# Performance work log

Hardware: AMD Instinct MI355X
Metric: run time of the kernel (lower is better)

Reference implementation:

```python
import jax, jax.numpy as jnp
import numpy as np

GROUP_SIZE = 128
N_BITS = 4
QMAX = 2 ** N_BITS - 1
NUM_EXPERTS = 8
HIDDEN = 2048
INTER = 768
NUM_ROT = 4
T_TOKENS = 4096
TOP_K = 2


def _make_pairs(rng, n_rot, in_feat):
    # intra-group permutation per rotation (valid disjoint Givens pairs)
    n_groups = in_feat // GROUP_SIZE
    return np.stack([
        np.concatenate([rng.permutation(GROUP_SIZE) for _ in range(n_groups)])
        for _ in range(n_rot)
    ]).astype(np.int32)


def _round_ste(x):
    return x + jax.lax.stop_gradient(jnp.round(x) - x)


def _rotate(W, pairs, angles):
    # W: [N, in_feat]; pairs: [R, in_feat] intra-group perm; angles: [R, in_feat//2]
    in_feat = W.shape[1]
    base = (jnp.arange(in_feat) // GROUP_SIZE) * GROUP_SIZE
    for r in range(pairs.shape[0]):
        abs_idx = base + pairs[r]
        i_idx = abs_idx[0::2]
        j_idx = abs_idx[1::2]
        c = jnp.cos(angles[r])
        s = jnp.sin(angles[r])
        wi = W[:, i_idx]
        wj = W[:, j_idx]
        W = W.at[:, i_idx].set(c * wi - s * wj).at[:, j_idx].set(s * wi + c * wj)
    return W


def _fake_quant(W):
    # groupwise asymmetric min-max fake quantization with STE rounding
    shape = W.shape
    wg = W.reshape(-1, GROUP_SIZE)
    wmax = wg.max(axis=-1, keepdims=True)
    wmin = wg.min(axis=-1, keepdims=True)
    scale = jnp.clip(wmax - wmin, 1e-5, None) / QMAX
    zero = jnp.round(-wmin / scale)
    q = jnp.clip(_round_ste(wg / scale) + zero, 0.0, float(QMAX))
    return ((q - zero) * scale).reshape(shape)


def _pseudo_quantize(W3, pairs, angles, ch_scales):
    # scale -> rotate -> fake-quant -> inverse rotate (reversed order, -angles) -> unscale
    E, O, In = W3.shape
    W = W3.reshape(-1, In) * ch_scales
    W = _rotate(W, pairs, angles)
    W = _fake_quant(W)
    W = _rotate(W, pairs[::-1], -angles[::-1])
    return (W / ch_scales).reshape(E, O, In)


def setup_inputs() -> dict:
    key = jax.random.key(0)
    ks = jax.random.split(key, 8)
    rng = np.random.default_rng(0)
    hidden_states = jax.random.normal(ks[0], (T_TOKENS, HIDDEN), jnp.float32)
    top_k_index = jax.random.randint(ks[1], (T_TOKENS, TOP_K), 0, NUM_EXPERTS, jnp.int32)
    logits = jax.random.normal(ks[2], (T_TOKENS, TOP_K), jnp.float32)
    top_k_weights = jax.nn.softmax(logits, axis=-1)
    gate_up_weight = jax.random.normal(ks[3], (NUM_EXPERTS, 2 * INTER, HIDDEN), jnp.float32) * 0.02
    down_weight = jax.random.normal(ks[4], (NUM_EXPERTS, HIDDEN, INTER), jnp.float32) * 0.02
    gate_up_pairs = jnp.asarray(_make_pairs(rng, NUM_ROT, HIDDEN))
    down_pairs = jnp.asarray(_make_pairs(rng, NUM_ROT, INTER))
    gate_up_angles = jax.random.normal(ks[5], (NUM_ROT, HIDDEN // 2), jnp.float32) * 0.1
    down_angles = jax.random.normal(ks[6], (NUM_ROT, INTER // 2), jnp.float32) * 0.1
    k7, k8 = jax.random.split(ks[7])
    gate_up_channel_scales = jax.random.uniform(k7, (1, HIDDEN), jnp.float32, 0.5, 1.5)
    down_channel_scales = jax.random.uniform(k8, (1, INTER), jnp.float32, 0.5, 1.5)
    return {
        "hidden_states": hidden_states,
        "top_k_index": top_k_index,
        "top_k_weights": top_k_weights,
        "gate_up_weight": gate_up_weight,
        "down_weight": down_weight,
        "gate_up_pairs": gate_up_pairs,
        "gate_up_angles": gate_up_angles,
        "down_pairs": down_pairs,
        "down_angles": down_angles,
        "gate_up_channel_scales": gate_up_channel_scales,
        "down_channel_scales": down_channel_scales,
    }


def reference(hidden_states, top_k_index, top_k_weights, gate_up_weight, down_weight,
              gate_up_pairs, gate_up_angles, down_pairs, down_angles,
              gate_up_channel_scales, down_channel_scales):
    # dequantize expert weights
    gup = _pseudo_quantize(gate_up_weight, gate_up_pairs, gate_up_angles, gate_up_channel_scales)  # [E,2I,H]
    dwn = _pseudo_quantize(down_weight, down_pairs, down_angles, down_channel_scales)              # [E,H,I]
    T = hidden_states.shape[0]
    E = gup.shape[0]
    # dense dispatch: all experts for all tokens (E small), combined by routing weights
    h = jnp.einsum('th,eoh->teo', hidden_states, gup)          # [T,E,2I]
    gate, up = jnp.split(h, 2, axis=-1)
    inter = jax.nn.silu(gate) * up                              # [T,E,I]
    y = jnp.einsum('tei,ehi->teh', inter, dwn)                  # [T,E,H]
    combine = jnp.zeros((T, E), hidden_states.dtype)
    combine = combine.at[jnp.arange(T)[:, None], top_k_index].add(top_k_weights)
    return jnp.einsum('teh,te->th', y, combine)
```

## Files before the change

### kernel.cpp

```cpp
#include <hip/hip_runtime.h>

#define T_TOKENS 4096
#define HIDDEN   2048
#define INTERM   768
#define NE       8
#define NPAIR    8192
#define NROT     4
#define MAXT     40

typedef __bf16 bf16x8 __attribute__((ext_vector_type(8)));
typedef float  f32x4  __attribute__((ext_vector_type(4)));

__device__ __forceinline__ unsigned short f2bf(float f) {
  unsigned u = __float_as_uint(f);
  u += 0x7fffu + ((u >> 16) & 1u);
  return (unsigned short)(u >> 16);
}

__device__ __forceinline__ void async16(const void* g, void* l) {
  __builtin_amdgcn_global_load_lds((const __attribute__((address_space(1))) void*)g,
                                   (__attribute__((address_space(3))) void*)l, 16, 0, 0);
}

__global__ void k_hist(const int* __restrict__ idx, int* __restrict__ cnt) {
  const int t = blockIdx.x * 256 + threadIdx.x;
  if (t < NPAIR) atomicAdd(&cnt[idx[t]], 1);
}

__global__ void k_scan(const int* __restrict__ cnt, int* __restrict__ off,
                       int* __restrict__ cur, int* __restrict__ tmap,
                       int* __restrict__ nv) {
  if (threadIdx.x == 0) {
    int a = 0, tt = 0;
    for (int e = 0; e < NE; ++e) {
      off[e] = a; cur[e] = 0;
      const int c = cnt[e];
      for (int m = 0; m < c; m += 256) tmap[tt++] = (e << 16) | (m >> 8);
      a += c;
    }
    nv[0] = tt;
    for (; tt < MAXT; ++tt) tmap[tt] = -1;
  }
}

__global__ void k_scatter(const int* __restrict__ idx, const float* __restrict__ wts,
                          const int* __restrict__ off, int* __restrict__ cur,
                          int* __restrict__ pt, float* __restrict__ pw) {
  const int t = blockIdx.x * 256 + threadIdx.x;
  if (t < NPAIR) {
    const int e = idx[t];
    const int pos = off[e] + atomicAdd(&cur[e], 1);
    pt[pos] = t;
    pw[pos] = wts[t];
  }
}

__global__ void k_tbl(const int* __restrict__ gp, const float* __restrict__ ga,
                      const int* __restrict__ dp, const float* __restrict__ da,
                      const float* __restrict__ gch, const float* __restrict__ dch,
                      float4* __restrict__ tg, float4* __restrict__ td,
                      float* __restrict__ grch, float* __restrict__ drch) {
  const int t = blockIdx.x * 256 + threadIdx.x;
  if (t < NROT * (HIDDEN / 2)) {
    const int r = t >> 10, s = t & 1023;
    const int grp = s >> 6;
    const int i = gp[r * HIDDEN + 2 * s], j = gp[r * HIDDEN + 2 * s + 1];
    const float a = ga[r * (HIDDEN / 2) + s];
    const float c = cosf(a), sn = sinf(a);
    tg[(grp * NROT + r) * 128 + i] = make_float4(c, -sn, __int_as_float(j), 0.f);
    tg[(grp * NROT + r) * 128 + j] = make_float4(c,  sn, __int_as_float(i), 0.f);
  }
  if (t < NROT * (INTERM / 2)) {
    const int r = t / (INTERM / 2), s = t - r * (INTERM / 2);
    const int grp = s >> 6;
    const int i = dp[r * INTERM + 2 * s], j = dp[r * INTERM + 2 * s + 1];
    const float a = da[r * (INTERM / 2) + s];
    const float c = cosf(a), sn = sinf(a);
    td[(grp * NROT + r) * 128 + i] = make_float4(c, -sn, __int_as_float(j), 0.f);
    td[(grp * NROT + r) * 128 + j] = make_float4(c,  sn, __int_as_float(i), 0.f);
  }
  if (t < HIDDEN) grch[t] = 1.0f / gch[t];
  if (t < INTERM) drch[t] = 1.0f / dch[t];
}

#define FWD_ROT(tl, v0, v1)                                                     \
  _Pragma("unroll")                                                             \
  for (int r = 0; r < NROT; ++r) {                                              \
    const float4 e0 = tl[r * 128 + l];                                          \
    const float4 e1 = tl[r * 128 + 64 + l];                                     \
    const int p0 = __float_as_int(e0.z), p1 = __float_as_int(e1.z);             \
    const int a0 = (p0 & 63) << 2, a1 = (p1 & 63) << 2;                         \
    _Pragma("unroll")                                                           \
    for (int q = 0; q < 4; ++q) {                                               \
      const int x0 = __float_as_int(v0[q]), x1 = __float_as_int(v1[q]);         \
      const float lo0 = __int_as_float(__builtin_amdgcn_ds_bpermute(a0, x0));   \
      const float hi0 = __int_as_float(__builtin_amdgcn_ds_bpermute(a0, x1));   \
      const float lo1 = __int_as_float(__builtin_amdgcn_ds_bpermute(a1, x0));   \
      const float hi1 = __int_as_float(__builtin_amdgcn_ds_bpermute(a1, x1));   \
      const float op0 = (p0 & 64) ? hi0 : lo0;                                  \
      const float op1 = (p1 & 64) ? hi1 : lo1;                                  \
      {                                                                         \
        _Pragma("clang fp contract(off)")                                       \
        v0[q] = e0.x * v0[q] + e0.y * op0;                                      \
        v1[q] = e1.x * v1[q] + e1.y * op1;                                      \
      }                                                                         \
    }                                                                           \
  }

__global__ __launch_bounds__(256) void k_quant(
    const float* __restrict__ W, const float4* __restrict__ tbl,
    const float* __restrict__ ch, unsigned short* __restrict__ out, int In, int G) {
  __shared__ float4 tl[NROT * 128];
  const int wv = threadIdx.x >> 6, l = threadIdx.x & 63;
  const int g = blockIdx.x % G;
  const int rowblk = blockIdx.x / G;
  const int row0 = rowblk * 16 + wv * 4;
  const int colbase = g << 7;
  tl[threadIdx.x]       = tbl[(size_t)g * NROT * 128 + threadIdx.x];
  tl[256 + threadIdx.x] = tbl[(size_t)g * NROT * 128 + 256 + threadIdx.x];
  __syncthreads();
  const float c0 = ch[colbase + l], c1 = ch[colbase + 64 + l];
  float v0[4], v1[4];
#pragma unroll
  for (int q = 0; q < 4; ++q) {
#pragma clang fp contract(off)
    const float* Wr = W + (size_t)(row0 + q) * In + colbase;
    v0[q] = Wr[l] * c0;
    v1[q] = Wr[64 + l] * c1;
  }
  FWD_ROT(tl, v0, v1)
#pragma unroll
  for (int q = 0; q < 4; ++q) {
    float mn = fminf(v0[q], v1[q]), mx = fmaxf(v0[q], v1[q]);
#pragma unroll
    for (int o = 32; o > 0; o >>= 1) {
      mn = fminf(mn, __shfl_xor(mn, o));
      mx = fmaxf(mx, __shfl_xor(mx, o));
    }
    {
#pragma clang fp contract(off)
      const float scale = fmaxf(mx - mn, 1e-5f) / 15.0f;
      const float zero = rintf(-mn / scale);
      const float q0 = fminf(fmaxf(rintf(v0[q] / scale) + zero, 0.0f), 15.0f);
      const float q1 = fminf(fmaxf(rintf(v1[q] / scale) + zero, 0.0f), 15.0f);
      v0[q] = (q0 - zero) * scale;
      v1[q] = (q1 - zero) * scale;
    }
  }
#pragma unroll
  for (int q = 0; q < 4; ++q) {
    unsigned short* Or = out + (size_t)(row0 + q) * In + colbase;
    Or[l]      = f2bf(v0[q]);
    Or[64 + l] = f2bf(v1[q]);
  }
}

__global__ __launch_bounds__(256) void k_rotx(
    const float* __restrict__ X, const float* __restrict__ rch,
    const float4* __restrict__ tbl, unsigned short* __restrict__ out) {
  __shared__ float4 tl[NROT * 128];
  const int wv = threadIdx.x >> 6, l = threadIdx.x & 63;
  const int g = blockIdx.x % 16;
  const int rowblk = blockIdx.x / 16;
  const int row0 = rowblk * 16 + wv * 4;
  const int colbase = g << 7;
  tl[threadIdx.x]       = tbl[(size_t)g * NROT * 128 + threadIdx.x];
  tl[256 + threadIdx.x] = tbl[(size_t)g * NROT * 128 + 256 + threadIdx.x];
  __syncthreads();
  const float i0 = rch[colbase + l], i1 = rch[colbase + 64 + l];
  float v0[4], v1[4];
#pragma unroll
  for (int q = 0; q < 4; ++q) {
    const float* Xr = X + (size_t)(row0 + q) * HIDDEN + colbase;
    v0[q] = Xr[l] * i0;
    v1[q] = Xr[64 + l] * i1;
  }
  FWD_ROT(tl, v0, v1)
#pragma unroll
  for (int q = 0; q < 4; ++q) {
    unsigned short* Or = out + (size_t)(row0 + q) * HIDDEN + colbase;
    Or[l]      = f2bf(v0[q]);
    Or[64 + l] = f2bf(v1[q]);
  }
}

__global__ __launch_bounds__(256) void k_silu2(
    const float* __restrict__ h, const float* __restrict__ pw,
    const float* __restrict__ rch, const float4* __restrict__ tbl,
    unsigned short* __restrict__ out) {
  __shared__ float4 tl[NROT * 128];
  const int wv = threadIdx.x >> 6, l = threadIdx.x & 63;
  const int g = blockIdx.x % 6;
  const int rowblk = blockIdx.x / 6;
  const int row0 = rowblk * 16 + wv * 4;
  const int colbase = g << 7;
  tl[threadIdx.x]       = tbl[(size_t)g * NROT * 128 + threadIdx.x];
  tl[256 + threadIdx.x] = tbl[(size_t)g * NROT * 128 + 256 + threadIdx.x];
  __syncthreads();
  const float i0 = rch[colbase + l], i1 = rch[colbase + 64 + l];
  float v0[4], v1[4];
#pragma unroll
  for (int q = 0; q < 4; ++q) {
    const int row = row0 + q;
    const float wgt = pw[row];
    const float* hr = h + (size_t)row * 1536 + colbase;
    const float g0 = hr[l], g1 = hr[64 + l];
    const float u0 = hr[768 + l], u1 = hr[768 + 64 + l];
    v0[q] = g0 / (1.0f + expf(-g0)) * u0 * wgt * i0;
    v1[q] = g1 / (1.0f + expf(-g1)) * u1 * wgt * i1;
  }
  FWD_ROT(tl, v0, v1)
#pragma unroll
  for (int q = 0; q < 4; ++q) {
    unsigned short* Or = out + (size_t)(row0 + q) * INTERM + colbase;
    Or[l]      = f2bf(v0[q]);
    Or[64 + l] = f2bf(v1[q]);
  }
}

template <int MODE>
__launch_bounds__(512, 2)
__global__ void k_gemm(const unsigned short* __restrict__ A,
                       const unsigned short* __restrict__ Bw,
                       float* __restrict__ C,
                       const int* __restrict__ pt,
                       const int* __restrict__ off,
                       const int* __restrict__ cnt,
                       const int* __restrict__ tmap,
                       const int* __restrict__ nv) {
  constexpr int K = MODE ? INTERM : HIDDEN;
  constexpr int N = MODE ? HIDDEN : 2 * INTERM;
  constexpr int XW = MODE ? 8 : 6;
  constexpr int NT = K / 64;

  const int hw  = blockIdx.x + XW * blockIdx.y;
  const int xcd = hw & 7;
  const int pos = hw >> 3;
  const int nvalid = nv[0];
  const int q8 = nvalid >> 3, r8 = nvalid & 7;
  const int rs = q8 + (xcd < r8 ? 1 : 0);
  const int y0 = xcd * q8 + (xcd < r8 ? xcd : r8);
  if (pos >= rs * XW) return;
  const int xg = pos % XW;
  const int yg = y0 + pos / XW;
  const int tm = tmap[yg];
  if (tm < 0) return;
  const int e = tm >> 16;
  const int m0 = (tm & 0xffff) << 8;
  const int count = cnt[e];
  const int seg = off[e];
  const int n0 = xg * 256;
  const unsigned short* Be = Bw + (size_t)e * N * K;

  __shared__ unsigned short lds[65536];

  const int tid = threadIdx.x;
  const int w = tid >> 6, l = tid & 63;
  const int wm = w >> 2, wn = w & 3;
  const int w512 = w * 512;

  const int sr = tid >> 2;
  const int cs = (((tid & 3) ^ ((tid >> 3) & 3))) * 8;
  int pA0 = m0 + sr;        if (pA0 > count - 1) pA0 = count - 1;
  int pA1 = m0 + sr + 128;  if (pA1 > count - 1) pA1 = count - 1;
  size_t arow0, arow1;
  if (MODE == 0) { arow0 = (size_t)(pt[seg + pA0] >> 1); arow1 = (size_t)(pt[seg + pA1] >> 1); }
  else           { arow0 = (size_t)(seg + pA0); arow1 = (size_t)(seg + pA1); }
  const unsigned short* paS0 = A + arow0 * K + cs;
  const unsigned short* paS1 = A + arow1 * K + cs;
  const unsigned short* pbS0 = Be + (size_t)(n0 + sr) * K + cs;
  const unsigned short* pbS1 = Be + (size_t)(n0 + sr + 128) * K + cs;

  const int cswz  = ((l >> 4) ^ (((l & 15) >> 1) & 3)) * 8;
  const int abase = (wm * 128 + (l & 15)) * 32 + cswz;
  const int bbase = (wn * 64  + (l & 15)) * 32 + cswz + 16384;

  f32x4 acc[8][4];
#pragma unroll
  for (int i = 0; i < 8; ++i)
#pragma unroll
    for (int j = 0; j < 4; ++j) acc[i][j] = (f32x4)0.0f;

#define STG_A(dst, koff) do { \
    async16(paS0 + (koff), &lds[(dst) + w512]); \
    async16(paS1 + (koff), &lds[(dst) + 4096 + w512]); } while (0)
#define STG_B(dst, koff) do { \
    async16(pbS0 + (koff), &lds[(dst) + w512]); \
    async16(pbS1 + (koff), &lds[(dst) + 4096 + w512]); } while (0)

  STG_A(0,     0);  STG_B(16384,       0);
  STG_A(8192,  32); STG_B(16384+8192,  32);
  STG_A(32768, 64); STG_B(32768+16384, 64);
  asm volatile("s_waitcnt vmcnt(4)" ::: "memory");
  __builtin_amdgcn_s_barrier();

  for (int t = 0; t < NT; ++t) {
    const int base = (t & 1) << 15;
    const int alt  = base ^ 32768;
    const int k1 = (t + 1) * 64, k2 = (t + 2) * 64;
    bf16x8 a[4], bq[4];

#pragma unroll
    for (int ii = 0; ii < 4; ++ii) a[ii]  = *(const bf16x8*)&lds[base + abase + ii * 512];
#pragma unroll
    for (int j = 0; j < 4; ++j)    bq[j]  = *(const bf16x8*)&lds[base + bbase + j * 512];
    if (t + 1 < NT) STG_A(alt + 8192, k1 + 32);
    __builtin_amdgcn_s_barrier();
    asm volatile("s_waitcnt lgkmcnt(0)" ::: "memory");
    __builtin_amdgcn_sched_barrier(0);
    __builtin_amdgcn_s_setprio(1);
#pragma unroll
    for (int ii = 0; ii < 4; ++ii)
#pragma unroll
      for (int j = 0; j < 4; ++j)
        acc[ii][j] = __builtin_amdgcn_mfma_f32_16x16x32_bf16(a[ii], bq[j], acc[ii][j], 0, 0, 0);
    __builtin_amdgcn_s_setprio(0);
    __builtin_amdgcn_s_barrier();

#pragma unroll
    for (int ii = 0; ii < 4; ++ii) a[ii] = *(const bf16x8*)&lds[base + abase + (4 + ii) * 512];
    if (t + 1 < NT) STG_B(alt + 16384 + 8192, k1 + 32);
    __builtin_amdgcn_s_barrier();
    asm volatile("s_waitcnt lgkmcnt(0)" ::: "memory");
    __builtin_amdgcn_sched_barrier(0);
    __builtin_amdgcn_s_setprio(1);
#pragma unroll
    for (int ii = 0; ii < 4; ++ii)
#pragma unroll
      for (int j = 0; j < 4; ++j)
        acc[4 + ii][j] = __builtin_amdgcn_mfma_f32_16x16x32_bf16(a[ii], bq[j], acc[4 + ii][j], 0, 0, 0);
    __builtin_amdgcn_s_setprio(0);
    __builtin_amdgcn_s_barrier();

#pragma unroll
    for (int ii = 0; ii < 4; ++ii) a[ii] = *(const bf16x8*)&lds[base + 8192 + abase + ii * 512];
#pragma unroll
    for (int j = 0; j < 4; ++j)    bq[j] = *(const bf16x8*)&lds[base + 8192 + bbase + j * 512];
    if (t + 2 < NT) STG_A(base, k2);
    __builtin_amdgcn_s_barrier();
    asm volatile("s_waitcnt lgkmcnt(0)" ::: "memory");
    __builtin_amdgcn_sched_barrier(0);
    __builtin_amdgcn_s_setprio(1);
#pragma unroll
    for (int ii = 0; ii < 4; ++ii)
#pragma unroll
      for (int j = 0; j < 4; ++j)
        acc[ii][j] = __builtin_amdgcn_mfma_f32_16x16x32_bf16(a[ii], bq[j], acc[ii][j], 0, 0, 0);
    __builtin_amdgcn_s_setprio(0);
    __builtin_amdgcn_s_barrier();

#pragma unroll
    for (int ii = 0; ii < 4; ++ii) a[ii] = *(const bf16x8*)&lds[base + 8192 + abase + (4 + ii) * 512];
    if (t + 2 < NT) STG_B(base + 16384, k2);
    __builtin_amdgcn_s_barrier();
    asm volatile("s_waitcnt lgkmcnt(0)" ::: "memory");
    __builtin_amdgcn_sched_barrier(0);
    __builtin_amdgcn_s_setprio(1);
#pragma unroll
    for (int ii = 0; ii < 4; ++ii)
#pragma unroll
      for (int j = 0; j < 4; ++j)
        acc[4 + ii][j] = __builtin_amdgcn_mfma_f32_16x16x32_bf16(a[ii], bq[j], acc[4 + ii][j], 0, 0, 0);
    __builtin_amdgcn_s_setprio(0);
    if (t + 1 < NT) {
      if (t + 1 == NT - 1) asm volatile("s_waitcnt vmcnt(0)" ::: "memory");
      else                 asm volatile("s_waitcnt vmcnt(4)" ::: "memory");
    }
    __builtin_amdgcn_s_barrier();
  }
#undef STG_A
#undef STG_B

  const int mb = wm * 128 + (l >> 4) * 4;
  const int nb = n0 + wn * 64 + (l & 15);
#pragma unroll
  for (int i = 0; i < 8; ++i) {
#pragma unroll
    for (int j = 0; j < 4; ++j) {
#pragma unroll
      for (int r = 0; r < 4; ++r) {
        const int mm = m0 + mb + i * 16 + r;
        if (mm < count) {
          const int nn = nb + j * 16;
          if (MODE == 0) {
            C[(size_t)(seg + mm) * N + nn] = acc[i][j][r];
          } else {
            C[(size_t)pt[seg + mm] * N + nn] = acc[i][j][r];
          }
        }
      }
    }
  }
}

__global__ __launch_bounds__(256) void k_combine(const float4* __restrict__ y,
                                                 float4* __restrict__ out) {
  const int t = blockIdx.x;
  const float4* y0 = y + (size_t)(2 * t) * (HIDDEN / 4);
  const float4* y1 = y + (size_t)(2 * t + 1) * (HIDDEN / 4);
  float4* o = out + (size_t)t * (HIDDEN / 4);
#pragma unroll
  for (int q = 0; q < 2; ++q) {
    const int c = threadIdx.x + q * 256;
    const float4 a = y0[c], b = y1[c];
    o[c] = make_float4(a.x + b.x, a.y + b.y, a.z + b.z, a.w + b.w);
  }
}

extern "C" void kernel_launch(void* const* d_in, const int* in_sizes, int n_in,
                              void* d_out, int out_size, void* d_ws, size_t ws_size,
                              hipStream_t stream) {
  const float* hs  = (const float*)d_in[0];
  const int*   tki = (const int*)d_in[1];
  const float* tkw = (const float*)d_in[2];
  const float* guw = (const float*)d_in[3];
  const float* dww = (const float*)d_in[4];
  const int*   gupr= (const int*)d_in[5];
  const float* gua = (const float*)d_in[6];
  const int*   dwp = (const int*)d_in[7];
  const float* dwa = (const float*)d_in[8];
  const float* gus = (const float*)d_in[9];
  const float* dwsc= (const float*)d_in[10];
  float* out = (float*)d_out;
  char* ws = (char*)d_ws;

  unsigned short* gup_bf = (unsigned short*)(ws + 0);
  unsigned short* dwn_bf = (unsigned short*)(ws + 50331648);
  unsigned short* x_bf   = (unsigned short*)(ws + 75497472);
  float*          hbuf   = (float*)(ws + 92274688);
  unsigned short* interb = (unsigned short*)(ws + 142606336);
  float*          ybuf   = (float*)(ws + 75497472);
  int*            pt     = (int*)(ws + 155189248);
  float*          pw     = (float*)(ws + 155222016);
  int*            cnt    = (int*)(ws + 155254784);
  int*            off    = cnt + 8;
  int*            cur    = cnt + 16;
  int*            tmap   = cnt + 24;
  int*            nv     = cnt + 120;
  float4*         tg     = (float4*)(ws + 155258880);
  float4*         td     = (float4*)(ws + 155389952);
  float*          grch   = (float*)(ws + 155439104);
  float*          drch   = (float*)(ws + 155447296);

  (void)hipMemsetAsync(cnt, 0, 32, stream);

  k_hist<<<32, 256, 0, stream>>>(tki, cnt);
  k_scan<<<1, 64, 0, stream>>>(cnt, off, cur, tmap, nv);
  k_scatter<<<32, 256, 0, stream>>>(tki, tkw, off, cur, pt, pw);
  k_tbl<<<16, 256, 0, stream>>>(gupr, gua, dwp, dwa, gus, dwsc, tg, td, grch, drch);
  k_rotx<<<4096, 256, 0, stream>>>(hs, grch, tg, x_bf);
  k_quant<<<12288, 256, 0, stream>>>(guw, tg, gus, gup_bf, HIDDEN, 16);
  k_quant<<<6144, 256, 0, stream>>>(dww, td, dwsc, dwn_bf, INTERM, 6);
  k_gemm<0><<<dim3(6, MAXT), 512, 0, stream>>>(x_bf, gup_bf, hbuf, pt, off, cnt, tmap, nv);
  k_silu2<<<3072, 256, 0, stream>>>(hbuf, pw, drch, td, interb);
  k_gemm<1><<<dim3(8, MAXT), 512, 0, stream>>>(interb, dwn_bf, ybuf, pt, off, cnt, tmap, nv);
  k_combine<<<T_TOKENS, 256, 0, stream>>>((const float4*)ybuf, (float4*)out);
}
```

Baseline: 538.3 us.

## Add specialized down-projection GEMM with 256x128 tiles and XCD-aware block mapping

Replaces the generic templated down-projection GEMM with a dedicated kernel that uses narrower N tiles (128 columns, 16 column blocks), double-buffered async global-to-LDS loads with a swizzled layout, and a block index remap that spreads row tiles across the eight XCDs. The aim is to raise the number of concurrent blocks and improve L2 locality for the small-K (768) down GEMM. Narrower N tiles mean the A tile is reloaded more often, adding global traffic in exchange for better occupancy and balance.

```diff
diff --git a/kernel.cpp b/kernel.cpp
--- a/kernel.cpp
+++ b/kernel.cpp
@@ -393,6 +393,107 @@
   }
 }
 
+__launch_bounds__(512, 4)
+__global__ void k_gemm1(const unsigned short* __restrict__ A,
+                        const unsigned short* __restrict__ Bw,
+                        float* __restrict__ C,
+                        const int* __restrict__ pt,
+                        const int* __restrict__ off,
+                        const int* __restrict__ cnt,
+                        const int* __restrict__ tmap,
+                        const int* __restrict__ nv) {
+  constexpr int K = INTERM;
+  constexpr int N = HIDDEN;
+  constexpr int XW = 16;
+  constexpr int NT = K / 32;
+
+  const int hw  = blockIdx.x + XW * blockIdx.y;
+  const int xcd = hw & 7;
+  const int pos = hw >> 3;
+  const int nvalid = nv[0];
+  const int q8 = nvalid >> 3, r8 = nvalid & 7;
+  const int rs = q8 + (xcd < r8 ? 1 : 0);
+  const int y0 = xcd * q8 + (xcd < r8 ? xcd : r8);
+  if (pos >= rs * XW) return;
+  const int xg = pos % XW;
+  const int yg = y0 + pos / XW;
+  const int tm = tmap[yg];
+  if (tm < 0) return;
+  const int e = tm >> 16;
+  const int m0 = (tm & 0xffff) << 8;
+  const int count = cnt[e];
+  const int seg = off[e];
+  const int n0 = xg * 128;
+  const unsigned short* Be = Bw + (size_t)e * N * K;
+
+  __shared__ unsigned short lds[24576];
+
+  const int tid = threadIdx.x;
+  const int w = tid >> 6, l = tid & 63;
+  const int wm = w >> 1, wn = w & 1;
+  const int w512 = w * 512;
+
+  const int sr = tid >> 2;
+  const int cs = ((tid & 3) ^ ((tid >> 3) & 3)) * 8;
+  int pA0 = m0 + sr;        if (pA0 > count - 1) pA0 = count - 1;
+  int pA1 = m0 + sr + 128;  if (pA1 > count - 1) pA1 = count - 1;
+  const unsigned short* paS0 = A + (size_t)(seg + pA0) * K + cs;
+  const unsigned short* paS1 = A + (size_t)(seg + pA1) * K + cs;
+  const unsigned short* pbS0 = Be + (size_t)(n0 + sr) * K + cs;
+
+  const int cswz  = ((l >> 4) ^ (((l & 15) >> 1) & 3)) * 8;
+  const int abase = (wm * 64 + (l & 15)) * 32 + cswz;
+  const int bbase = 8192 + (wn * 64 + (l & 15)) * 32 + cswz;
+
+  f32x4 acc[4][4];
+#pragma unroll
+  for (int i = 0; i < 4; ++i)
+#pragma unroll
+    for (int j = 0; j < 4; ++j) acc[i][j] = (f32x4)0.0f;
+
+#define STG1(b, koff) do {                                   \
+    async16(paS0 + (koff), &lds[(b) * 12288 + w512]);        \
+    async16(paS1 + (koff), &lds[(b) * 12288 + 4096 + w512]); \
+    async16(pbS0 + (koff), &lds[(b) * 12288 + 8192 + w512]); \
+  } while (0)
+
+  STG1(0, 0);
+  int buf = 0;
+  for (int t = 0; t < NT; ++t) {
+    __syncthreads();
+    if (t + 1 < NT) STG1(buf ^ 1, (t + 1) * 32);
+    const int lb = buf * 12288;
+    bf16x8 a[4], bq[4];
+#pragma unroll
+    for (int i = 0; i < 4; ++i) a[i]  = *(const bf16x8*)&lds[lb + abase + i * 512];
+#pragma unroll
+    for (int j = 0; j < 4; ++j) bq[j] = *(const bf16x8*)&lds[lb + bbase + j * 512];
+#pragma unroll
+    for (int i = 0; i < 4; ++i)
+#pragma unroll
+      for (int j = 0; j < 4; ++j)
+        acc[i][j] = __builtin_amdgcn_mfma_f32_16x16x32_bf16(a[i], bq[j], acc[i][j], 0, 0, 0);
+    buf ^= 1;
+  }
+#undef STG1
+
+  const int mb = wm * 64 + (l >> 4) * 4;
+  const int nb = n0 + wn * 64 + (l & 15);
+#pragma unroll
+  for (int i = 0; i < 4; ++i) {
+#pragma unroll
+    for (int j = 0; j < 4; ++j) {
+#pragma unroll
+      for (int r = 0; r < 4; ++r) {
+        const int mm = m0 + mb + i * 16 + r;
+        if (mm < count) {
+          C[(size_t)pt[seg + mm] * N + nb + j * 16] = acc[i][j][r];
+        }
+      }
+    }
+  }
+}
+
 __global__ __launch_bounds__(256) void k_combine(const float4* __restrict__ y,
                                                  float4* __restrict__ out) {
   const int t = blockIdx.x;
@@ -453,6 +554,6 @@
   k_quant<<<6144, 256, 0, stream>>>(dww, td, dwsc, dwn_bf, INTERM, 6);
   k_gemm<0><<<dim3(6, MAXT), 512, 0, stream>>>(x_bf, gup_bf, hbuf, pt, off, cnt, tmap, nv);
   k_silu2<<<3072, 256, 0, stream>>>(hbuf, pw, drch, td, interb);
-  k_gemm<1><<<dim3(8, MAXT), 512, 0, stream>>>(interb, dwn_bf, ybuf, pt, off, cnt, tmap, nv);
+  k_gemm1<<<dim3(16, MAXT), 512, 0, stream>>>(interb, dwn_bf, ybuf, pt, off, cnt, tmap, nv);
   k_combine<<<T_TOKENS, 256, 0, stream>>>((const float4*)ybuf, (float4*)out);
 }
```

Result: faster. 519.1 us (-3.6%).
